# Optimization experiments

Measured on AMD Instinct MI355X. Metric: run time of the kernel, lower is better.

Reference implementation:

```python
import jax, jax.numpy as jnp
import numpy as np

B, E, LC, LE, D = 32, 8, 256, 512, 256   # batch, evi_num, claim_len, evidence_len, emb_dim
OUT, H = 128, 1                          # attention hidden dim, head_num
NEG = -1e18


def setup_inputs() -> dict:
    key = jax.random.key(0)
    ks = jax.random.split(key, 8)
    claim = jax.random.normal(ks[0], (B, E, LC, D), jnp.float32)
    evidence = jax.random.normal(ks[1], (B, E, LE, D), jnp.float32)
    claim_len_mask = jax.random.randint(ks[2], (B, E, 1, LC), 0, 2).astype(jnp.int32)
    evidence_len_mask = jax.random.randint(ks[3], (B, E, 1, LE), 0, 2).astype(jnp.int32)
    s2d = 1.0 / np.sqrt(2 * D)
    so = 1.0 / np.sqrt(OUT)
    W1 = jax.random.normal(ks[4], (2 * D, OUT), jnp.float32) * s2d  # torch W1.weight.T
    w2 = jax.random.normal(ks[5], (OUT, H), jnp.float32) * so
    W2 = jax.random.normal(ks[6], (2 * D, OUT), jnp.float32) * s2d
    w1 = jax.random.normal(ks[7], (OUT, H), jnp.float32) * so
    return {"claim": claim, "claim_len_mask": claim_len_mask,
            "evidence": evidence, "evidence_len_mask": evidence_len_mask,
            "W1": W1, "w2": w2, "W2": W2, "w1": w1}


def _pooled_attend(seq, seq_mask, pooled, W, w):
    # seq: (B,E,L,D), pooled: (B,E,1,D), W: (2D,OUT), w: (OUT,H)
    # cat([seq, pooled_expanded]) @ W  ==  seq @ W[:D] + pooled @ W[D:]  (broadcast)
    h = jnp.tanh(seq @ W[:D] + pooled @ W[D:])          # (B,E,L,OUT)
    att = h @ w                                          # (B,E,L,H)
    mask = jnp.swapaxes(seq_mask, -1, -2).astype(bool)   # (B,E,L,1), broadcast over H
    att = jnp.where(mask, att, NEG)
    scores = jax.nn.softmax(att, axis=-2)                # softmax over L
    out = jnp.einsum('belh,beld->behd', scores, seq)     # (B,E,H,D)
    return out.reshape(out.shape[0], out.shape[1], 1, -1)  # (B,E,1,H*D)


def reference(claim, claim_len_mask, evidence, evidence_len_mask, W1, w2, W2, w1):
    c_mean = jnp.mean(claim, axis=-2, keepdims=True)     # (B,E,1,D)
    e_hat = _pooled_attend(evidence, evidence_len_mask, c_mean, W1, w2)
    e_mean = jnp.mean(evidence, axis=-2, keepdims=True)  # (B,E,1,D)
    c_hat = _pooled_attend(claim, claim_len_mask, e_mean, W2, w1)
    return c_hat, e_hat
```

## Files before the change

### kernel.cpp

```cpp
#include <hip/hip_runtime.h>
#include <hip/hip_bf16.h>
#include <math.h>

#define BE   256
#define DIM  256
#define OUTD 128
#define LCL  256
#define LEV  512
#define NEGV -1e18f

typedef short  bf16x8  __attribute__((ext_vector_type(8)));
typedef float  floatx4 __attribute__((ext_vector_type(4)));

union BF1 { __hip_bfloat16 h; unsigned short u; };
union BF2 { __hip_bfloat162 h; unsigned int u; };

__device__ __forceinline__ float fast_tanh(float x) {
    float xc = fminf(fmaxf(x, -15.f), 15.f);
    float e = __expf(2.f * xc);
    return (e - 1.f) * __builtin_amdgcn_rcpf(e + 1.f);
}

__global__ __launch_bounds__(256) void k_meanprep(
    const float* __restrict__ claim, const float* __restrict__ evidence,
    const float* __restrict__ W1, const float* __restrict__ W2,
    float* __restrict__ partial,
    unsigned short* __restrict__ WT1, unsigned short* __restrict__ WT2)
{
    const int b = blockIdx.x;
    const int t = threadIdx.x;
    if (b >= 3072) {
        const int idx = b - 3072;
        const int side = idx >> 7;
        const int n = idx & 127;
        const float* W = side ? W2 : W1;
        unsigned short* WT = side ? WT2 : WT1;
        BF1 c; c.h = __float2bfloat16(W[(size_t)t * OUTD + n]);
        WT[n * DIM + t] = c.u;
        return;
    }
    const int pair = b / 12;
    const int chunk = b % 12;
    const float* src = (chunk < 4)
        ? claim + ((size_t)pair * LCL + chunk * 64) * DIM
        : evidence + ((size_t)pair * LEV + (chunk - 4) * 64) * DIM;
    float s = 0.f;
#pragma unroll
    for (int r = 0; r < 64; ++r) s += src[r * DIM + t];
    partial[(size_t)b * DIM + t] = s;
}

__global__ __launch_bounds__(512) void k_redbias(
    const float* __restrict__ partial,
    const float* __restrict__ W1, const float* __restrict__ W2,
    float* __restrict__ bias_e, float* __restrict__ bias_c)
{
    const int pair = blockIdx.x;
    const int t = threadIdx.x;
    __shared__ float sm[2][DIM];
    __shared__ float sb[2][2][OUTD];
    if (t < 256) {
        float s = 0.f;
#pragma unroll
        for (int j = 0; j < 4; ++j) s += partial[((size_t)pair * 12 + j) * DIM + t];
        sm[0][t] = s * (1.f / LCL);
    } else {
        const int t2 = t - 256;
        float s = 0.f;
#pragma unroll
        for (int j = 4; j < 12; ++j) s += partial[((size_t)pair * 12 + j) * DIM + t2];
        sm[1][t2] = s * (1.f / LEV);
    }
    __syncthreads();
    const int side = t >> 8, o = t & 127, dh = (t >> 7) & 1;
    const float* W = side ? W2 : W1;
    const float* m = sm[side];
    float s = 0.f;
#pragma unroll 8
    for (int i = 0; i < 128; ++i) {
        const int d = dh * 128 + i;
        s += m[d] * W[(size_t)(DIM + d) * OUTD + o];
    }
    sb[side][dh][o] = s;
    __syncthreads();
    if (t < 256) {
        const int sd = t >> 7, oo = t & 127;
        const float bv = sb[sd][0][oo] + sb[sd][1][oo];
        (sd ? bias_c : bias_e)[pair * OUTD + oo] = bv;
    }
}

template <int L>
__global__ __launch_bounds__(256) void k_att(
    const float* __restrict__ seq, const unsigned short* __restrict__ WT,
    const float* __restrict__ wvec, const float* __restrict__ bias,
    float* __restrict__ att)
{
    constexpr int SAPC = 136;
    __shared__ unsigned short sA[128 * SAPC];
    __shared__ float sred[128][2];

    const int pair = blockIdx.x;
    const int rowbase = blockIdx.y * 128;
    const int t = threadIdx.x;
    const int lane = t & 63;
    const int wv = t >> 6;
    const int wrow = wv >> 1, wcolg = wv & 1;
    const int q = lane >> 4, c16 = lane & 15;

    const float4* sp4 = (const float4*)(seq + ((size_t)pair * L + rowbase) * DIM);

    floatx4 acc[4][4];
#pragma unroll
    for (int ra = 0; ra < 4; ++ra)
#pragma unroll
        for (int ct = 0; ct < 4; ++ct) acc[ra][ct] = (floatx4){0.f, 0.f, 0.f, 0.f};

    const unsigned short* wbase = WT + (size_t)(wcolg * 64 + c16) * DIM + q * 8;
    bf16x8 bcur[4], bnxt[4];
#pragma unroll
    for (int ct = 0; ct < 4; ++ct)
        bcur[ct] = *(const bf16x8*)(wbase + ct * 16 * DIM);

    for (int kc = 0; kc < 2; ++kc) {
        __syncthreads();
#pragma unroll
        for (int i = 0; i < 16; ++i) {
            const int idx = t + i * 256;
            const int row = idx >> 5;
            const int f4 = idx & 31;
            const float4 v = sp4[row * 64 + kc * 32 + f4];
            BF2 lo, hi;
            lo.h = __float22bfloat162_rn(make_float2(v.x, v.y));
            hi.h = __float22bfloat162_rn(make_float2(v.z, v.w));
            *(uint2*)&sA[row * SAPC + f4 * 4] = make_uint2(lo.u, hi.u);
        }
        __syncthreads();
#pragma unroll
        for (int ks4 = 0; ks4 < 4; ++ks4) {
            const int ks = kc * 4 + ks4;
            if (ks < 7) {
#pragma unroll
                for (int ct = 0; ct < 4; ++ct)
                    bnxt[ct] = *(const bf16x8*)(wbase + ct * 16 * DIM + (ks + 1) * 32);
            }
            bf16x8 af[4];
#pragma unroll
            for (int ra = 0; ra < 4; ++ra)
                af[ra] = *(const bf16x8*)&sA[(wrow * 64 + ra * 16 + c16) * SAPC + ks4 * 32 + q * 8];
#pragma unroll
            for (int ra = 0; ra < 4; ++ra)
#pragma unroll
                for (int ct = 0; ct < 4; ++ct)
                    acc[ra][ct] = __builtin_amdgcn_mfma_f32_16x16x32_bf16(af[ra], bcur[ct], acc[ra][ct], 0, 0, 0);
#pragma unroll
            for (int ct = 0; ct < 4; ++ct) bcur[ct] = bnxt[ct];
        }
    }

    float bc[4], wc[4];
#pragma unroll
    for (int ct = 0; ct < 4; ++ct) {
        const int col = wcolg * 64 + ct * 16 + c16;
        bc[ct] = bias[pair * OUTD + col];
        wc[ct] = wvec[col];
    }
#pragma unroll
    for (int ra = 0; ra < 4; ++ra) {
#pragma unroll
        for (int reg = 0; reg < 4; ++reg) {
            float s = 0.f;
#pragma unroll
            for (int ct = 0; ct < 4; ++ct)
                s += fast_tanh(acc[ra][ct][reg] + bc[ct]) * wc[ct];
#pragma unroll
            for (int off = 1; off < 16; off <<= 1) s += __shfl_xor(s, off, 64);
            if (c16 == 0)
                sred[wrow * 64 + ra * 16 + q * 4 + reg][wcolg] = s;
        }
    }
    __syncthreads();
    if (t < 128)
        att[(size_t)pair * L + rowbase + t] = sred[t][0] + sred[t][1];
}

template <int L>
__global__ __launch_bounds__(1024) void k_soft(
    const float* __restrict__ seq, const int* __restrict__ mask,
    const float* __restrict__ att, float* __restrict__ outp)
{
    const int pair = blockIdx.x;
    const int t = threadIdx.x;
    __shared__ float p[L];
    __shared__ float red[8];
    __shared__ float4 red2[16][64];

    float lmax = -INFINITY;
    if (t < 256) {
#pragma unroll
        for (int k = 0; k < L / 256; ++k) {
            const int i = t + k * 256;
            float a = att[(size_t)pair * L + i];
            a = mask[pair * L + i] ? a : NEGV;
            p[i] = a;
            lmax = fmaxf(lmax, a);
        }
#pragma unroll
        for (int off = 32; off > 0; off >>= 1) lmax = fmaxf(lmax, __shfl_xor(lmax, off, 64));
        if ((t & 63) == 0) red[t >> 6] = lmax;
    }
    __syncthreads();
    if (t < 256) {
        const float gmax = fmaxf(fmaxf(red[0], red[1]), fmaxf(red[2], red[3]));
        float lsum = 0.f;
#pragma unroll
        for (int k = 0; k < L / 256; ++k) {
            const int i = t + k * 256;
            const float e = expf(p[i] - gmax);
            p[i] = e;
            lsum += e;
        }
#pragma unroll
        for (int off = 32; off > 0; off >>= 1) lsum += __shfl_xor(lsum, off, 64);
        if ((t & 63) == 0) red[4 + (t >> 6)] = lsum;
    }
    __syncthreads();

    const int d4 = t & 63, lg = t >> 6;
    constexpr int LC = L / 16;
    const float4* sp4 = (const float4*)(seq + (size_t)pair * L * DIM);
    float4 o = make_float4(0.f, 0.f, 0.f, 0.f);
    for (int l = lg * LC; l < (lg + 1) * LC; ++l) {
        const float pl = p[l];
        const float4 v = sp4[l * 64 + d4];
        o.x += pl * v.x; o.y += pl * v.y; o.z += pl * v.z; o.w += pl * v.w;
    }
    red2[lg][d4] = o;
    __syncthreads();
    if (t < 64) {
        float4 s = make_float4(0.f, 0.f, 0.f, 0.f);
#pragma unroll
        for (int j = 0; j < 16; ++j) {
            const float4 v = red2[j][t];
            s.x += v.x; s.y += v.y; s.z += v.z; s.w += v.w;
        }
        const float inv = 1.f / (red[4] + red[5] + red[6] + red[7]);
        ((float4*)(outp + (size_t)pair * DIM))[t] =
            make_float4(s.x * inv, s.y * inv, s.z * inv, s.w * inv);
    }
}

extern "C" void kernel_launch(void* const* d_in, const int* in_sizes, int n_in,
                              void* d_out, int out_size, void* d_ws, size_t ws_size,
                              hipStream_t stream) {
    const float* claim    = (const float*)d_in[0];
    const int*   cmask    = (const int*)  d_in[1];
    const float* evidence = (const float*)d_in[2];
    const int*   emask    = (const int*)  d_in[3];
    const float* W1       = (const float*)d_in[4];
    const float* w2       = (const float*)d_in[5];
    const float* W2       = (const float*)d_in[6];
    const float* w1       = (const float*)d_in[7];
    float* out = (float*)d_out;

    float* ws = (float*)d_ws;
    float* partial = ws;
    float* bias_e  = partial + 3072 * DIM;
    float* bias_c  = bias_e + BE * OUTD;
    float* att_e   = bias_c + BE * OUTD;
    float* att_c   = att_e + BE * LEV;
    unsigned short* WT1 = (unsigned short*)(att_c + BE * LCL);
    unsigned short* WT2 = WT1 + OUTD * DIM;

    k_meanprep<<<3328, 256, 0, stream>>>(claim, evidence, W1, W2, partial, WT1, WT2);
    k_redbias<<<BE, 512, 0, stream>>>(partial, W1, W2, bias_e, bias_c);
    k_att<LEV><<<dim3(BE, 4), 256, 0, stream>>>(evidence, WT1, w2, bias_e, att_e);
    k_att<LCL><<<dim3(BE, 2), 256, 0, stream>>>(claim, WT2, w1, bias_c, att_c);
    k_soft<LEV><<<BE, 1024, 0, stream>>>(evidence, emask, att_e, out + BE * DIM);
    k_soft<LCL><<<BE, 1024, 0, stream>>>(claim, cmask, att_c, out);
}
```

Measured before the change: 344.9 us.

## Fuse attention scoring, softmax and pooling per pair; compute evidence mean inside

```diff
diff --git a/kernel.cpp b/kernel.cpp
--- a/kernel.cpp
+++ b/kernel.cpp
@@ -21,16 +21,16 @@
     return (e - 1.f) * __builtin_amdgcn_rcpf(e + 1.f);
 }
 
-__global__ __launch_bounds__(256) void k_meanprep(
-    const float* __restrict__ claim, const float* __restrict__ evidence,
+__global__ __launch_bounds__(256) void k_prep(
+    const float* __restrict__ claim,
     const float* __restrict__ W1, const float* __restrict__ W2,
-    float* __restrict__ partial,
+    float* __restrict__ cpart,
     unsigned short* __restrict__ WT1, unsigned short* __restrict__ WT2)
 {
     const int b = blockIdx.x;
     const int t = threadIdx.x;
-    if (b >= 3072) {
-        const int idx = b - 3072;
+    if (b >= 1024) {
+        const int idx = b - 1024;
         const int side = idx >> 7;
         const int n = idx & 127;
         const float* W = side ? W2 : W1;
@@ -39,199 +39,160 @@
         WT[n * DIM + t] = c.u;
         return;
     }
-    const int pair = b / 12;
-    const int chunk = b % 12;
-    const float* src = (chunk < 4)
-        ? claim + ((size_t)pair * LCL + chunk * 64) * DIM
-        : evidence + ((size_t)pair * LEV + (chunk - 4) * 64) * DIM;
-    float s = 0.f;
-#pragma unroll
-    for (int r = 0; r < 64; ++r) s += src[r * DIM + t];
-    partial[(size_t)b * DIM + t] = s;
-}
-
-__global__ __launch_bounds__(512) void k_redbias(
-    const float* __restrict__ partial,
-    const float* __restrict__ W1, const float* __restrict__ W2,
-    float* __restrict__ bias_e, float* __restrict__ bias_c)
+    __shared__ float4 red[4][64];
+    const int d4 = t & 63, rg = t >> 6;
+    const float4* sp4 = (const float4*)(claim + ((size_t)(b >> 2) * LCL + (b & 3) * 64) * DIM);
+    float4 a = make_float4(0.f, 0.f, 0.f, 0.f);
+#pragma unroll
+    for (int r = 0; r < 16; ++r) {
+        const float4 v = sp4[(rg * 16 + r) * 64 + d4];
+        a.x += v.x; a.y += v.y; a.z += v.z; a.w += v.w;
+    }
+    red[rg][d4] = a;
+    __syncthreads();
+    if (t < 64) {
+        float4 s = make_float4(0.f, 0.f, 0.f, 0.f);
+#pragma unroll
+        for (int j = 0; j < 4; ++j) {
+            const float4 v = red[j][t];
+            s.x += v.x; s.y += v.y; s.z += v.z; s.w += v.w;
+        }
+        ((float4*)(cpart + (size_t)b * DIM))[t] = s;
+    }
+}
+
+__global__ __launch_bounds__(256) void k_bias(
+    const float* __restrict__ src, int nchunks, float scale,
+    const float* __restrict__ W, float* __restrict__ bias)
 {
     const int pair = blockIdx.x;
     const int t = threadIdx.x;
-    __shared__ float sm[2][DIM];
-    __shared__ float sb[2][2][OUTD];
-    if (t < 256) {
-        float s = 0.f;
-#pragma unroll
-        for (int j = 0; j < 4; ++j) s += partial[((size_t)pair * 12 + j) * DIM + t];
-        sm[0][t] = s * (1.f / LCL);
-    } else {
-        const int t2 = t - 256;
-        float s = 0.f;
-#pragma unroll
-        for (int j = 4; j < 12; ++j) s += partial[((size_t)pair * 12 + j) * DIM + t2];
-        sm[1][t2] = s * (1.f / LEV);
-    }
-    __syncthreads();
-    const int side = t >> 8, o = t & 127, dh = (t >> 7) & 1;
-    const float* W = side ? W2 : W1;
-    const float* m = sm[side];
+    __shared__ float sm[DIM];
+    __shared__ float sb[2][OUTD];
     float s = 0.f;
+    for (int j = 0; j < nchunks; ++j)
+        s += src[((size_t)pair * nchunks + j) * DIM + t];
+    sm[t] = s * scale;
+    __syncthreads();
+    const int o = t & 127, dh = t >> 7;
+    float b = 0.f;
 #pragma unroll 8
     for (int i = 0; i < 128; ++i) {
         const int d = dh * 128 + i;
-        s += m[d] * W[(size_t)(DIM + d) * OUTD + o];
-    }
-    sb[side][dh][o] = s;
-    __syncthreads();
-    if (t < 256) {
-        const int sd = t >> 7, oo = t & 127;
-        const float bv = sb[sd][0][oo] + sb[sd][1][oo];
-        (sd ? bias_c : bias_e)[pair * OUTD + oo] = bv;
-    }
-}
-
-template <int L>
-__global__ __launch_bounds__(256) void k_att(
+        b += sm[d] * W[(size_t)(DIM + d) * OUTD + o];
+    }
+    sb[dh][o] = b;
+    __syncthreads();
+    if (t < 128) bias[pair * OUTD + t] = sb[0][t] + sb[1][t];
+}
+
+template <int L, bool MEAN>
+__global__ __launch_bounds__(512) void k_fused(
     const float* __restrict__ seq, const unsigned short* __restrict__ WT,
     const float* __restrict__ wvec, const float* __restrict__ bias,
-    float* __restrict__ att)
+    const int* __restrict__ mask, float* __restrict__ outp,
+    float* __restrict__ meanout)
 {
-    constexpr int SAPC = 136;
+    constexpr int SAPC = 264;
     __shared__ unsigned short sA[128 * SAPC];
-    __shared__ float sred[128][2];
+    __shared__ float satt[L];
+    __shared__ float sred8[8], ssum8[8];
+    __shared__ float4 red2[8][64];
 
     const int pair = blockIdx.x;
-    const int rowbase = blockIdx.y * 128;
     const int t = threadIdx.x;
-    const int lane = t & 63;
-    const int wv = t >> 6;
-    const int wrow = wv >> 1, wcolg = wv & 1;
+    const int lane = t & 63, w = t >> 6;
     const int q = lane >> 4, c16 = lane & 15;
-
-    const float4* sp4 = (const float4*)(seq + ((size_t)pair * L + rowbase) * DIM);
-
-    floatx4 acc[4][4];
-#pragma unroll
-    for (int ra = 0; ra < 4; ++ra)
-#pragma unroll
-        for (int ct = 0; ct < 4; ++ct) acc[ra][ct] = (floatx4){0.f, 0.f, 0.f, 0.f};
-
-    const unsigned short* wbase = WT + (size_t)(wcolg * 64 + c16) * DIM + q * 8;
-    bf16x8 bcur[4], bnxt[4];
-#pragma unroll
-    for (int ct = 0; ct < 4; ++ct)
-        bcur[ct] = *(const bf16x8*)(wbase + ct * 16 * DIM);
-
-    for (int kc = 0; kc < 2; ++kc) {
+    const int d4 = t & 63, lg = t >> 6;
+
+    const float4* sp4 = (const float4*)(seq + (size_t)pair * L * DIM);
+
+    float bc[8], wc[8];
+#pragma unroll
+    for (int ct = 0; ct < 8; ++ct) {
+        bc[ct] = bias[pair * OUTD + ct * 16 + c16];
+        wc[ct] = wvec[ct * 16 + c16];
+    }
+
+    float4 macc = make_float4(0.f, 0.f, 0.f, 0.f);
+
+    for (int tile = 0; tile < L / 128; ++tile) {
         __syncthreads();
 #pragma unroll
         for (int i = 0; i < 16; ++i) {
-            const int idx = t + i * 256;
-            const int row = idx >> 5;
-            const int f4 = idx & 31;
-            const float4 v = sp4[row * 64 + kc * 32 + f4];
+            const int row = (t + i * 512) >> 6;
+            const float4 v = sp4[(tile * 128 + row) * 64 + d4];
+            if (MEAN) { macc.x += v.x; macc.y += v.y; macc.z += v.z; macc.w += v.w; }
             BF2 lo, hi;
             lo.h = __float22bfloat162_rn(make_float2(v.x, v.y));
             hi.h = __float22bfloat162_rn(make_float2(v.z, v.w));
-            *(uint2*)&sA[row * SAPC + f4 * 4] = make_uint2(lo.u, hi.u);
-        }
-        __syncthreads();
-#pragma unroll
-        for (int ks4 = 0; ks4 < 4; ++ks4) {
-            const int ks = kc * 4 + ks4;
-            if (ks < 7) {
-#pragma unroll
-                for (int ct = 0; ct < 4; ++ct)
-                    bnxt[ct] = *(const bf16x8*)(wbase + ct * 16 * DIM + (ks + 1) * 32);
+            *(uint2*)&sA[row * SAPC + d4 * 4] = make_uint2(lo.u, hi.u);
+        }
+        __syncthreads();
+
+        floatx4 acc[8];
+#pragma unroll
+        for (int ct = 0; ct < 8; ++ct) acc[ct] = (floatx4){0.f, 0.f, 0.f, 0.f};
+#pragma unroll
+        for (int ks = 0; ks < 8; ++ks) {
+            const bf16x8 af = *(const bf16x8*)&sA[(w * 16 + c16) * SAPC + ks * 32 + q * 8];
+#pragma unroll
+            for (int ct = 0; ct < 8; ++ct) {
+                const bf16x8 bf = *(const bf16x8*)(WT + (size_t)(ct * 16 + c16) * DIM + ks * 32 + q * 8);
+                acc[ct] = __builtin_amdgcn_mfma_f32_16x16x32_bf16(af, bf, acc[ct], 0, 0, 0);
             }
-            bf16x8 af[4];
-#pragma unroll
-            for (int ra = 0; ra < 4; ++ra)
-                af[ra] = *(const bf16x8*)&sA[(wrow * 64 + ra * 16 + c16) * SAPC + ks4 * 32 + q * 8];
-#pragma unroll
-            for (int ra = 0; ra < 4; ++ra)
-#pragma unroll
-                for (int ct = 0; ct < 4; ++ct)
-                    acc[ra][ct] = __builtin_amdgcn_mfma_f32_16x16x32_bf16(af[ra], bcur[ct], acc[ra][ct], 0, 0, 0);
-#pragma unroll
-            for (int ct = 0; ct < 4; ++ct) bcur[ct] = bnxt[ct];
-        }
-    }
-
-    float bc[4], wc[4];
-#pragma unroll
-    for (int ct = 0; ct < 4; ++ct) {
-        const int col = wcolg * 64 + ct * 16 + c16;
-        bc[ct] = bias[pair * OUTD + col];
-        wc[ct] = wvec[col];
-    }
-#pragma unroll
-    for (int ra = 0; ra < 4; ++ra) {
+        }
 #pragma unroll
         for (int reg = 0; reg < 4; ++reg) {
             float s = 0.f;
 #pragma unroll
-            for (int ct = 0; ct < 4; ++ct)
-                s += fast_tanh(acc[ra][ct][reg] + bc[ct]) * wc[ct];
+            for (int ct = 0; ct < 8; ++ct)
+                s += fast_tanh(acc[ct][reg] + bc[ct]) * wc[ct];
 #pragma unroll
             for (int off = 1; off < 16; off <<= 1) s += __shfl_xor(s, off, 64);
             if (c16 == 0)
-                sred[wrow * 64 + ra * 16 + q * 4 + reg][wcolg] = s;
-        }
-    }
-    __syncthreads();
-    if (t < 128)
-        att[(size_t)pair * L + rowbase + t] = sred[t][0] + sred[t][1];
-}
-
-template <int L>
-__global__ __launch_bounds__(1024) void k_soft(
-    const float* __restrict__ seq, const int* __restrict__ mask,
-    const float* __restrict__ att, float* __restrict__ outp)
-{
-    const int pair = blockIdx.x;
-    const int t = threadIdx.x;
-    __shared__ float p[L];
-    __shared__ float red[8];
-    __shared__ float4 red2[16][64];
-
-    float lmax = -INFINITY;
-    if (t < 256) {
-#pragma unroll
-        for (int k = 0; k < L / 256; ++k) {
-            const int i = t + k * 256;
-            float a = att[(size_t)pair * L + i];
-            a = mask[pair * L + i] ? a : NEGV;
-            p[i] = a;
-            lmax = fmaxf(lmax, a);
-        }
-#pragma unroll
-        for (int off = 32; off > 0; off >>= 1) lmax = fmaxf(lmax, __shfl_xor(lmax, off, 64));
-        if ((t & 63) == 0) red[t >> 6] = lmax;
-    }
-    __syncthreads();
-    if (t < 256) {
-        const float gmax = fmaxf(fmaxf(red[0], red[1]), fmaxf(red[2], red[3]));
-        float lsum = 0.f;
-#pragma unroll
-        for (int k = 0; k < L / 256; ++k) {
-            const int i = t + k * 256;
-            const float e = expf(p[i] - gmax);
-            p[i] = e;
-            lsum += e;
-        }
-#pragma unroll
-        for (int off = 32; off > 0; off >>= 1) lsum += __shfl_xor(lsum, off, 64);
-        if ((t & 63) == 0) red[4 + (t >> 6)] = lsum;
-    }
-    __syncthreads();
-
-    const int d4 = t & 63, lg = t >> 6;
-    constexpr int LC = L / 16;
-    const float4* sp4 = (const float4*)(seq + (size_t)pair * L * DIM);
+                satt[tile * 128 + w * 16 + q * 4 + reg] = s;
+        }
+    }
+    __syncthreads();
+
+    if (MEAN) {
+        red2[lg][d4] = macc;
+        __syncthreads();
+        if (t < 64) {
+            float4 s = make_float4(0.f, 0.f, 0.f, 0.f);
+#pragma unroll
+            for (int j = 0; j < 8; ++j) {
+                const float4 v = red2[j][t];
+                s.x += v.x; s.y += v.y; s.z += v.z; s.w += v.w;
+            }
+            ((float4*)(meanout + (size_t)pair * DIM))[t] = s;
+        }
+        __syncthreads();
+    }
+
+    float a = -INFINITY;
+    if (t < L) a = mask[pair * L + t] ? satt[t] : NEGV;
+    float lmax = a;
+#pragma unroll
+    for (int off = 32; off > 0; off >>= 1) lmax = fmaxf(lmax, __shfl_xor(lmax, off, 64));
+    if (lane == 0) sred8[w] = lmax;
+    __syncthreads();
+    float gmax = -INFINITY;
+#pragma unroll
+    for (int j = 0; j < 8; ++j) gmax = fmaxf(gmax, sred8[j]);
+    float e = 0.f;
+    if (t < L) { e = __expf(a - gmax); satt[t] = e; }
+    float lsum = e;
+#pragma unroll
+    for (int off = 32; off > 0; off >>= 1) lsum += __shfl_xor(lsum, off, 64);
+    if (lane == 0) ssum8[w] = lsum;
+    __syncthreads();
+
+    constexpr int LC = L / 8;
     float4 o = make_float4(0.f, 0.f, 0.f, 0.f);
     for (int l = lg * LC; l < (lg + 1) * LC; ++l) {
-        const float pl = p[l];
+        const float pl = satt[l];
         const float4 v = sp4[l * 64 + d4];
         o.x += pl * v.x; o.y += pl * v.y; o.z += pl * v.z; o.w += pl * v.w;
     }
@@ -240,11 +201,13 @@
     if (t < 64) {
         float4 s = make_float4(0.f, 0.f, 0.f, 0.f);
 #pragma unroll
-        for (int j = 0; j < 16; ++j) {
+        for (int j = 0; j < 8; ++j) {
             const float4 v = red2[j][t];
             s.x += v.x; s.y += v.y; s.z += v.z; s.w += v.w;
         }
-        const float inv = 1.f / (red[4] + red[5] + red[6] + red[7]);
+        const float gsum = ssum8[0] + ssum8[1] + ssum8[2] + ssum8[3]
+                         + ssum8[4] + ssum8[5] + ssum8[6] + ssum8[7];
+        const float inv = 1.f / gsum;
         ((float4*)(outp + (size_t)pair * DIM))[t] =
             make_float4(s.x * inv, s.y * inv, s.z * inv, s.w * inv);
     }
@@ -264,18 +227,18 @@
     float* out = (float*)d_out;
 
     float* ws = (float*)d_ws;
-    float* partial = ws;
-    float* bias_e  = partial + 3072 * DIM;
-    float* bias_c  = bias_e + BE * OUTD;
-    float* att_e   = bias_c + BE * OUTD;
-    float* att_c   = att_e + BE * LEV;
-    unsigned short* WT1 = (unsigned short*)(att_c + BE * LCL);
+    float* cpart  = ws;
+    float* emean  = cpart + 1024 * DIM;
+    float* bias_e = emean + BE * DIM;
+    float* bias_c = bias_e + BE * OUTD;
+    unsigned short* WT1 = (unsigned short*)(bias_c + BE * OUTD);
     unsigned short* WT2 = WT1 + OUTD * DIM;
 
-    k_meanprep<<<3328, 256, 0, stream>>>(claim, evidence, W1, W2, partial, WT1, WT2);
-    k_redbias<<<BE, 512, 0, stream>>>(partial, W1, W2, bias_e, bias_c);
-    k_att<LEV><<<dim3(BE, 4), 256, 0, stream>>>(evidence, WT1, w2, bias_e, att_e);
-    k_att<LCL><<<dim3(BE, 2), 256, 0, stream>>>(claim, WT2, w1, bias_c, att_c);
-    k_soft<LEV><<<BE, 1024, 0, stream>>>(evidence, emask, att_e, out + BE * DIM);
-    k_soft<LCL><<<BE, 1024, 0, stream>>>(claim, cmask, att_c, out);
-}
+    k_prep<<<1280, 256, 0, stream>>>(claim, W1, W2, cpart, WT1, WT2);
+    k_bias<<<BE, 256, 0, stream>>>(cpart, 4, 1.f / LCL, W1, bias_e);
+    k_fused<LEV, true><<<BE, 512, 0, stream>>>(evidence, WT1, w2, bias_e, emask,
+                                               out + BE * DIM, emean);
+    k_bias<<<BE, 256, 0, stream>>>(emean, 1, 1.f / LEV, W2, bias_c);
+    k_fused<LCL, false><<<BE, 512, 0, stream>>>(claim, WT2, w1, bias_c, cmask,
+                                                out, nullptr);
+}
```

Measured after the change: 466.4 us. 1.35x slower.

## Merge claim/evidence launches and vectorize mean partial sums

Applied to the files above, without the earlier changes.

```diff
diff --git a/kernel.cpp b/kernel.cpp
--- a/kernel.cpp
+++ b/kernel.cpp
@@ -21,10 +21,10 @@
     return (e - 1.f) * __builtin_amdgcn_rcpf(e + 1.f);
 }
 
-__global__ __launch_bounds__(256) void k_meanprep(
+__global__ __launch_bounds__(256) void k_prep(
     const float* __restrict__ claim, const float* __restrict__ evidence,
     const float* __restrict__ W1, const float* __restrict__ W2,
-    float* __restrict__ partial,
+    float* __restrict__ cpart, float* __restrict__ epart,
     unsigned short* __restrict__ WT1, unsigned short* __restrict__ WT2)
 {
     const int b = blockIdx.x;
@@ -39,74 +39,84 @@
         WT[n * DIM + t] = c.u;
         return;
     }
-    const int pair = b / 12;
-    const int chunk = b % 12;
-    const float* src = (chunk < 4)
-        ? claim + ((size_t)pair * LCL + chunk * 64) * DIM
-        : evidence + ((size_t)pair * LEV + (chunk - 4) * 64) * DIM;
-    float s = 0.f;
-#pragma unroll
-    for (int r = 0; r < 64; ++r) s += src[r * DIM + t];
-    partial[(size_t)b * DIM + t] = s;
-}
-
-__global__ __launch_bounds__(512) void k_redbias(
-    const float* __restrict__ partial,
+    __shared__ float4 red[4][64];
+    const int d4 = t & 63, rg = t >> 6;
+    const float4* sp4;
+    float* dst;
+    if (b < 1024) {
+        sp4 = (const float4*)(claim + ((size_t)(b >> 2) * LCL + (b & 3) * 64) * DIM);
+        dst = cpart + (size_t)b * DIM;
+    } else {
+        const int idx = b - 1024;
+        sp4 = (const float4*)(evidence + ((size_t)(idx >> 3) * LEV + (idx & 7) * 64) * DIM);
+        dst = epart + (size_t)idx * DIM;
+    }
+    float4 a = make_float4(0.f, 0.f, 0.f, 0.f);
+#pragma unroll
+    for (int r = 0; r < 16; ++r) {
+        const float4 v = sp4[(rg * 16 + r) * 64 + d4];
+        a.x += v.x; a.y += v.y; a.z += v.z; a.w += v.w;
+    }
+    red[rg][d4] = a;
+    __syncthreads();
+    if (t < 64) {
+        float4 s = make_float4(0.f, 0.f, 0.f, 0.f);
+#pragma unroll
+        for (int j = 0; j < 4; ++j) {
+            const float4 v = red[j][t];
+            s.x += v.x; s.y += v.y; s.z += v.z; s.w += v.w;
+        }
+        ((float4*)dst)[t] = s;
+    }
+}
+
+__global__ __launch_bounds__(256) void k_bias(
+    const float* __restrict__ cpart, const float* __restrict__ epart,
     const float* __restrict__ W1, const float* __restrict__ W2,
     float* __restrict__ bias_e, float* __restrict__ bias_c)
 {
     const int pair = blockIdx.x;
+    const int side = blockIdx.y;
     const int t = threadIdx.x;
-    __shared__ float sm[2][DIM];
-    __shared__ float sb[2][2][OUTD];
-    if (t < 256) {
-        float s = 0.f;
-#pragma unroll
-        for (int j = 0; j < 4; ++j) s += partial[((size_t)pair * 12 + j) * DIM + t];
-        sm[0][t] = s * (1.f / LCL);
-    } else {
-        const int t2 = t - 256;
-        float s = 0.f;
-#pragma unroll
-        for (int j = 4; j < 12; ++j) s += partial[((size_t)pair * 12 + j) * DIM + t2];
-        sm[1][t2] = s * (1.f / LEV);
-    }
-    __syncthreads();
-    const int side = t >> 8, o = t & 127, dh = (t >> 7) & 1;
+    const float* src = side ? epart : cpart;
+    const int nch = side ? 8 : 4;
+    const float scale = side ? (1.f / LEV) : (1.f / LCL);
     const float* W = side ? W2 : W1;
-    const float* m = sm[side];
+    float* bias = side ? bias_c : bias_e;
+
+    __shared__ float sm[DIM];
+    __shared__ float sb[2][OUTD];
     float s = 0.f;
+    for (int j = 0; j < nch; ++j)
+        s += src[((size_t)pair * nch + j) * DIM + t];
+    sm[t] = s * scale;
+    __syncthreads();
+    const int o = t & 127, dh = t >> 7;
+    float b = 0.f;
 #pragma unroll 8
     for (int i = 0; i < 128; ++i) {
         const int d = dh * 128 + i;
-        s += m[d] * W[(size_t)(DIM + d) * OUTD + o];
-    }
-    sb[side][dh][o] = s;
-    __syncthreads();
-    if (t < 256) {
-        const int sd = t >> 7, oo = t & 127;
-        const float bv = sb[sd][0][oo] + sb[sd][1][oo];
-        (sd ? bias_c : bias_e)[pair * OUTD + oo] = bv;
-    }
+        b += sm[d] * W[(size_t)(DIM + d) * OUTD + o];
+    }
+    sb[dh][o] = b;
+    __syncthreads();
+    if (t < 128) bias[pair * OUTD + t] = sb[0][t] + sb[1][t];
 }
 
 template <int L>
-__global__ __launch_bounds__(256) void k_att(
+__device__ __forceinline__ void att_body(
     const float* __restrict__ seq, const unsigned short* __restrict__ WT,
     const float* __restrict__ wvec, const float* __restrict__ bias,
-    float* __restrict__ att)
+    float* __restrict__ att, int pair, int tile,
+    unsigned short* __restrict__ sA, float (*__restrict__ sred)[2])
 {
     constexpr int SAPC = 136;
-    __shared__ unsigned short sA[128 * SAPC];
-    __shared__ float sred[128][2];
-
-    const int pair = blockIdx.x;
-    const int rowbase = blockIdx.y * 128;
     const int t = threadIdx.x;
     const int lane = t & 63;
     const int wv = t >> 6;
     const int wrow = wv >> 1, wcolg = wv & 1;
     const int q = lane >> 4, c16 = lane & 15;
+    const int rowbase = tile * 128;
 
     const float4* sp4 = (const float4*)(seq + ((size_t)pair * L + rowbase) * DIM);
 
@@ -184,19 +194,31 @@
         att[(size_t)pair * L + rowbase + t] = sred[t][0] + sred[t][1];
 }
 
+__global__ __launch_bounds__(256) void k_att(
+    const float* __restrict__ claim, const float* __restrict__ evidence,
+    const unsigned short* __restrict__ WT1, const unsigned short* __restrict__ WT2,
+    const float* __restrict__ w2v, const float* __restrict__ w1v,
+    const float* __restrict__ bias_e, const float* __restrict__ bias_c,
+    float* __restrict__ att_e, float* __restrict__ att_c)
+{
+    __shared__ unsigned short sA[128 * 136];
+    __shared__ float sred[128][2];
+    if (blockIdx.y < 4)
+        att_body<LEV>(evidence, WT1, w2v, bias_e, att_e, blockIdx.x, blockIdx.y, sA, sred);
+    else
+        att_body<LCL>(claim, WT2, w1v, bias_c, att_c, blockIdx.x, blockIdx.y - 4, sA, sred);
+}
+
 template <int L>
-__global__ __launch_bounds__(1024) void k_soft(
+__device__ __forceinline__ void soft_body(
     const float* __restrict__ seq, const int* __restrict__ mask,
-    const float* __restrict__ att, float* __restrict__ outp)
-{
-    const int pair = blockIdx.x;
+    const float* __restrict__ att, float* __restrict__ outp, int pair,
+    float* __restrict__ p, float* __restrict__ red, float4 (*__restrict__ red2)[64])
+{
     const int t = threadIdx.x;
-    __shared__ float p[L];
-    __shared__ float red[8];
-    __shared__ float4 red2[16][64];
-
-    float lmax = -INFINITY;
+
     if (t < 256) {
+        float lmax = -INFINITY;
 #pragma unroll
         for (int k = 0; k < L / 256; ++k) {
             const int i = t + k * 256;
@@ -216,7 +238,7 @@
 #pragma unroll
         for (int k = 0; k < L / 256; ++k) {
             const int i = t + k * 256;
-            const float e = expf(p[i] - gmax);
+            const float e = __expf(p[i] - gmax);
             p[i] = e;
             lsum += e;
         }
@@ -230,6 +252,7 @@
     constexpr int LC = L / 16;
     const float4* sp4 = (const float4*)(seq + (size_t)pair * L * DIM);
     float4 o = make_float4(0.f, 0.f, 0.f, 0.f);
+#pragma unroll 4
     for (int l = lg * LC; l < (lg + 1) * LC; ++l) {
         const float pl = p[l];
         const float4 v = sp4[l * 64 + d4];
@@ -248,6 +271,21 @@
         ((float4*)(outp + (size_t)pair * DIM))[t] =
             make_float4(s.x * inv, s.y * inv, s.z * inv, s.w * inv);
     }
+}
+
+__global__ __launch_bounds__(1024) void k_soft(
+    const float* __restrict__ claim, const float* __restrict__ evidence,
+    const int* __restrict__ cmask, const int* __restrict__ emask,
+    const float* __restrict__ att_e, const float* __restrict__ att_c,
+    float* __restrict__ out)
+{
+    __shared__ float p[LEV];
+    __shared__ float red[8];
+    __shared__ float4 red2[16][64];
+    if (blockIdx.x < BE)
+        soft_body<LCL>(claim, cmask, att_c, out, blockIdx.x, p, red, red2);
+    else
+        soft_body<LEV>(evidence, emask, att_e, out + BE * DIM, blockIdx.x - BE, p, red, red2);
 }
 
 extern "C" void kernel_launch(void* const* d_in, const int* in_sizes, int n_in,
@@ -264,18 +302,18 @@
     float* out = (float*)d_out;
 
     float* ws = (float*)d_ws;
-    float* partial = ws;
-    float* bias_e  = partial + 3072 * DIM;
-    float* bias_c  = bias_e + BE * OUTD;
-    float* att_e   = bias_c + BE * OUTD;
-    float* att_c   = att_e + BE * LEV;
+    float* cpart  = ws;
+    float* epart  = cpart + 1024 * DIM;
+    float* bias_e = epart + 2048 * DIM;
+    float* bias_c = bias_e + BE * OUTD;
+    float* att_e  = bias_c + BE * OUTD;
+    float* att_c  = att_e + BE * LEV;
     unsigned short* WT1 = (unsigned short*)(att_c + BE * LCL);
     unsigned short* WT2 = WT1 + OUTD * DIM;
 
-    k_meanprep<<<3328, 256, 0, stream>>>(claim, evidence, W1, W2, partial, WT1, WT2);
-    k_redbias<<<BE, 512, 0, stream>>>(partial, W1, W2, bias_e, bias_c);
-    k_att<LEV><<<dim3(BE, 4), 256, 0, stream>>>(evidence, WT1, w2, bias_e, att_e);
-    k_att<LCL><<<dim3(BE, 2), 256, 0, stream>>>(claim, WT2, w1, bias_c, att_c);
-    k_soft<LEV><<<BE, 1024, 0, stream>>>(evidence, emask, att_e, out + BE * DIM);
-    k_soft<LCL><<<BE, 1024, 0, stream>>>(claim, cmask, att_c, out);
-}
+    k_prep<<<3328, 256, 0, stream>>>(claim, evidence, W1, W2, cpart, epart, WT1, WT2);
+    k_bias<<<dim3(BE, 2), 256, 0, stream>>>(cpart, epart, W1, W2, bias_e, bias_c);
+    k_att<<<dim3(BE, 6), 256, 0, stream>>>(claim, evidence, WT1, WT2, w2, w1,
+                                           bias_e, bias_c, att_e, att_c);
+    k_soft<<<512, 1024, 0, stream>>>(claim, evidence, cmask, emask, att_e, att_c, out);
+}
```

New measurement: 353.9 us. 2.6% more time.
